# Kernel optimization log

Hardware: AMD Instinct MI355X
Metric: run time of the kernel (lower is better)

Reference implementation:

```python
import jax, jax.numpy as jnp
import numpy as np

B, N, C = 4, 1024, 1024
H, TD, MULT = 16, 256, 4
HD = C // H
MAX_LEN = 1024
EPS = 1e-5


def _layer_norm(x, g, b):
    m = jnp.mean(x, axis=-1, keepdims=True)
    v = jnp.mean((x - m) ** 2, axis=-1, keepdims=True)
    return (x - m) / jnp.sqrt(v + EPS) * g + b


def _skew(x):
    # x: [B,H,N,M] -> pad left on last dim, reshape, drop first row -> [B,H,N,M]
    b, h, n, m = x.shape
    x = jnp.pad(x, ((0, 0), (0, 0), (0, 0), (1, 0)))
    x = x.reshape(b, h, m + 1, n)
    return x[:, :, 1:, :]


def setup_inputs() -> dict:
    key = jax.random.key(0)
    ks = jax.random.split(key, 16)
    s = 0.02
    return {
        "x": jax.random.normal(ks[0], (B, N, C), jnp.float32),
        "t": jax.random.normal(ks[1], (B, TD), jnp.float32),
        "ln1_g": jnp.ones((C,), jnp.float32),
        "ln1_b": jnp.zeros((C,), jnp.float32),
        "qkv_w": jax.random.normal(ks[2], (C, 3 * C), jnp.float32) * s,
        "qkv_b": jnp.zeros((3 * C,), jnp.float32),
        "time_w": jax.random.normal(ks[3], (TD, 3 * C), jnp.float32) * s,
        "time_b": jnp.zeros((3 * C,), jnp.float32),
        "out_w": jax.random.normal(ks[4], (C, C), jnp.float32) * s,
        "out_b": jnp.zeros((C,), jnp.float32),
        "Er": jax.random.normal(ks[5], (MAX_LEN, HD), jnp.float32) * s,
        "ln2_g": jnp.ones((C,), jnp.float32),
        "ln2_b": jnp.zeros((C,), jnp.float32),
        "ff1_w": jax.random.normal(ks[6], (C, MULT * C), jnp.float32) * s,
        "ff1_b": jnp.zeros((MULT * C,), jnp.float32),
        "ff2_w": jax.random.normal(ks[7], (MULT * C, C), jnp.float32) * s,
        "ff2_b": jnp.zeros((C,), jnp.float32),
    }


def reference(x, t, ln1_g, ln1_b, qkv_w, qkv_b, time_w, time_b, out_w, out_b,
              Er, ln2_g, ln2_b, ff1_w, ff1_b, ff2_w, ff2_b):
    # ---- attention branch ----
    xn = _layer_norm(x, ln1_g, ln1_b)
    qkv = (xn @ qkv_w + qkv_b).reshape(B, N, 3, H, HD).transpose(2, 0, 3, 1, 4)
    q, k, v = qkv[0], qkv[1], qkv[2]  # [B,H,N,HD]
    tqkv = (t @ time_w + time_b).reshape(B, 1, 3, H, HD).transpose(2, 0, 3, 1, 4)
    q = q + tqkv[0]
    k = k + tqkv[1]
    v = v + tqkv[2]
    Er_n = Er[MAX_LEN - N:]  # [N,HD]
    rel = jnp.einsum('bhnd,md->bhnm', q, Er_n)
    rel = _skew(rel)
    scale = HD ** -0.5
    attn = jnp.einsum('bhnd,bhmd->bhnm', q, k) * scale + rel
    attn = jax.nn.softmax(attn, axis=-1)
    out = jnp.einsum('bhnm,bhmd->bhnd', attn, v)
    out = out.transpose(0, 2, 1, 3).reshape(B, N, C)
    x = x + (out @ out_w + out_b)
    # ---- FFN branch ----
    h = _layer_norm(x, ln2_g, ln2_b)
    h = jax.nn.gelu(h @ ff1_w + ff1_b, approximate=False)
    x = x + (h @ ff2_w + ff2_b)
    return x
```

## Files before the change

### kernel.cpp

```cpp
#include <hip/hip_runtime.h>
#include <hip/hip_bf16.h>

typedef __attribute__((ext_vector_type(8))) short short8;
typedef __attribute__((ext_vector_type(4))) float f32x4;
typedef __attribute__((ext_vector_type(16))) float f32x16;

#define DEV __device__ __forceinline__

DEV float bf2f(ushort u){ union { float f; unsigned int i; } x; x.i = ((unsigned int)u)<<16; return x.f; }
DEV ushort f2bf(float f){ union { float fl; unsigned int i; } x; x.fl = f; unsigned int r = x.i + 0x7fffu + ((x.i>>16)&1u); return (ushort)(r>>16); }

DEV void gl2lds16(const ushort* g, ushort* l){
  __builtin_amdgcn_global_load_lds((const __attribute__((address_space(1))) void*)g,
                                   (__attribute__((address_space(3))) void*)l, 16, 0, 0);
}
DEV f32x16 mfma32(short8 a, short8 b, f32x16 c){
  return __builtin_amdgcn_mfma_f32_32x32x16_bf16(a, b, c, 0, 0, 0);
}
DEV uint cvtpk(float lo, float hi){
  uint r; asm("v_cvt_pk_bf16_f32 %0, %1, %2" : "=v"(r) : "v"(lo), "v"(hi));
  return r;
}
DEV uint q8(float v){
  float c = fminf(fmaxf(v, -127.f), 127.f);
  return ((uint)(int)rintf(c)) & 255u;
}

__global__ void cvt_f2b(const float* __restrict__ in, ushort* __restrict__ out, int n){
  int i = blockIdx.x*blockDim.x + threadIdx.x;
  int stride = gridDim.x*blockDim.x;
  for (; i < n; i += stride) out[i] = f2bf(in[i]);
}

__global__ __launch_bounds__(256) void wt_cvt(const float* __restrict__ in, ushort* __restrict__ out,
                                              int K, int N, int ldk){
  const int n0 = blockIdx.x*64, k0 = blockIdx.y*64;
  __shared__ float T[64][65];
  const int tid = threadIdx.x;
  const int r = tid>>4, c = (tid&15)*4;
  #pragma unroll
  for (int p=0;p<4;p++){
    float4 v = *(const float4*)&in[(size_t)(k0 + p*16 + r)*N + n0 + c];
    T[p*16+r][c+0]=v.x; T[p*16+r][c+1]=v.y; T[p*16+r][c+2]=v.z; T[p*16+r][c+3]=v.w;
  }
  __syncthreads();
  #pragma unroll
  for (int p=0;p<4;p++){
    int n = p*16 + r;
    ushort u0 = f2bf(T[c+0][n]), u1 = f2bf(T[c+1][n]), u2 = f2bf(T[c+2][n]), u3 = f2bf(T[c+3][n]);
    ushort4 u = make_ushort4(u0,u1,u2,u3);
    *(ushort4*)&out[(size_t)(n0+n)*ldk + k0 + c] = u;
  }
}

__global__ __launch_bounds__(256) void vt_k(const ushort* __restrict__ qkv, ushort* __restrict__ vt){
  const int bh = blockIdx.y; const int b = bh>>4, h = bh&15;
  const int n0 = blockIdx.x*64;
  __shared__ ushort T[64][66];
  const int tid = threadIdx.x;
  const int r = tid>>3, c8 = (tid&7)*8;
  #pragma unroll
  for (int p=0;p<2;p++){
    int row = p*32 + r;
    short8 v = *(const short8*)&qkv[(size_t)(b*1024 + n0 + row)*3200 + 2048 + h*64 + c8];
    #pragma unroll
    for (int i=0;i<8;i++) T[row][c8+i] = ((ushort*)&v)[i];
  }
  __syncthreads();
  #pragma unroll
  for (int p=0;p<2;p++){
    int d = p*32 + r;
    union { ushort u[8]; short8 v; } o;
    #pragma unroll
    for (int i=0;i<8;i++) o.u[i] = T[c8+i][d];
    *(short8*)&vt[(size_t)(bh*64 + d)*1152 + n0 + c8] = o.v;
  }
}

__global__ __launch_bounds__(256) void ln_rows(const float* __restrict__ in,
                                               const float* __restrict__ g,
                                               const float* __restrict__ bta,
                                               ushort* __restrict__ out, int ldo){
  int row = blockIdx.x; int tid = threadIdx.x;
  const float* x = in + (size_t)row*1024;
  float v[4]; float s = 0.f;
  #pragma unroll
  for (int i=0;i<4;i++){ v[i] = x[tid + 256*i]; s += v[i]; }
  __shared__ float rbuf[256];
  rbuf[tid] = s; __syncthreads();
  for (int off=128; off>0; off>>=1){ if (tid<off) rbuf[tid]+=rbuf[tid+off]; __syncthreads(); }
  float mean = rbuf[0] * (1.f/1024.f);
  __syncthreads();
  float s2 = 0.f;
  #pragma unroll
  for (int i=0;i<4;i++){ float d=v[i]-mean; s2 += d*d; }
  rbuf[tid] = s2; __syncthreads();
  for (int off=128; off>0; off>>=1){ if (tid<off) rbuf[tid]+=rbuf[tid+off]; __syncthreads(); }
  float var = rbuf[0] * (1.f/1024.f);
  float rstd = rsqrtf(var + 1e-5f);
  #pragma unroll
  for (int i=0;i<4;i++){ int c = tid+256*i; out[(size_t)row*ldo+c] = f2bf((v[i]-mean)*rstd*g[c]+bta[c]); }
}

__global__ __launch_bounds__(256) void tq_gemm2(const float* __restrict__ t, const float* __restrict__ tw,
                                                const float* __restrict__ tb, float* __restrict__ tq){
  const int tid = threadIdx.x;
  const int j = blockIdx.x*64 + (tid & 63);
  const int sl = tid >> 6;
  float acc[4] = {0.f,0.f,0.f,0.f};
  for (int k = sl*64; k < sl*64+64; ++k){
    float wv = tw[(size_t)k*3072 + j];
    #pragma unroll
    for (int b=0;b<4;b++) acc[b] = fmaf(t[b*256+k], wv, acc[b]);
  }
  __shared__ float red[4][4][64];
  #pragma unroll
  for (int b=0;b<4;b++) red[sl][b][tid&63] = acc[b];
  __syncthreads();
  if (sl == 0){
    #pragma unroll
    for (int b=0;b<4;b++)
      tq[b*3072 + j] = red[0][b][tid&63] + red[1][b][tid&63] + red[2][b][tid&63] + red[3][b][tid&63] + tb[j];
  }
}

template<int EPI, int TN>
__global__ __launch_bounds__(256) void gemm4(
    const ushort* __restrict__ A, const ushort* __restrict__ Bt,
    const float* __restrict__ bias, const float* __restrict__ extra,
    ushort* __restrict__ outb, float* __restrict__ outf,
    int K, int lda, int ldb, int ldo, int lde, int nbx)
{
  constexpr int NJ = TN/32;
  __shared__ __align__(16) ushort Al[2][128*32];
  __shared__ __align__(16) ushort Bl[2][TN*32];
  const int nwg = gridDim.x, cpx = nwg >> 3;
  const int bid = blockIdx.x;
  const int swz = (bid & 7)*cpx + (bid >> 3);
  const int m0 = (swz / nbx)*128, n0 = (swz % nbx)*TN;
  const int tid = threadIdx.x, lane = tid & 63, wid = tid >> 6;
  const int wm = (wid&1)*64, wn = (wid>>1)*(TN/2);
  const int l15 = lane&15, l4 = lane>>4;
  f32x4 acc[4][NJ];
  #pragma unroll
  for (int i=0;i<4;i++)
    #pragma unroll
    for (int jx=0;jx<NJ;jx++){ acc[i][jx][0]=0.f; acc[i][jx][1]=0.f; acc[i][jx][2]=0.f; acc[i][jx][3]=0.f; }
  const ushort* a0p = A + (size_t)(m0 + (tid>>2))*lda + (tid&3)*8;
  const ushort* a1p = A + (size_t)(m0 + 64 + (tid>>2))*lda + (tid&3)*8;
  const ushort* b0p = Bt + (size_t)(n0 + (tid>>2))*ldb + (tid&3)*8;
  const ushort* b1p = nullptr;
  if constexpr (TN==128) b1p = Bt + (size_t)(n0 + 64 + (tid>>2))*ldb + (tid&3)*8;
  const int lsl = tid*8, lsh = (tid+256)*8;

  gl2lds16(a0p, &Al[0][lsl]);
  gl2lds16(a1p, &Al[0][lsh]);
  gl2lds16(b0p, &Bl[0][lsl]);
  if constexpr (TN==128) gl2lds16(b1p, &Bl[0][lsh]);
  __syncthreads();

  const int nk = K >> 5;
  for (int it=0; it<nk; ++it){
    const int cur = it & 1;
    ushort* Ac = Al[cur];  ushort* Bc = Bl[cur];
    if (it+1 < nk){
      const int k1 = (it+1) << 5;
      gl2lds16(a0p + k1, &Al[cur^1][lsl]);
      gl2lds16(a1p + k1, &Al[cur^1][lsh]);
      gl2lds16(b0p + k1, &Bl[cur^1][lsl]);
      if constexpr (TN==128) gl2lds16(b1p + k1, &Bl[cur^1][lsh]);
    }
    short8 af[4], bfr[NJ];
    #pragma unroll
    for (int mi=0;mi<4;mi++) af[mi]  = *(const short8*)&Ac[(wm + mi*16 + l15)*32 + l4*8];
    #pragma unroll
    for (int nj=0;nj<NJ;nj++) bfr[nj] = *(const short8*)&Bc[(wn + nj*16 + l15)*32 + l4*8];
    #pragma unroll
    for (int mi=0;mi<4;mi++)
      #pragma unroll
      for (int nj=0;nj<NJ;nj++)
        acc[mi][nj] = __builtin_amdgcn_mfma_f32_16x16x32_bf16(af[mi], bfr[nj], acc[mi][nj], 0,0,0);
    __syncthreads();
  }
  #pragma unroll
  for (int mi=0;mi<4;mi++)
    #pragma unroll
    for (int nj=0;nj<NJ;nj++)
      #pragma unroll
      for (int j=0;j<4;j++){
        int row = m0 + wm + mi*16 + l4*4 + j;
        int col = n0 + wn + nj*16 + l15;
        float v = acc[mi][nj][j] + bias[col];
        if constexpr (EPI==0){ v += extra[(size_t)(row>>10)*lde + col]; outb[(size_t)row*ldo+col] = f2bf(v); }
        else if constexpr (EPI==1){ v += extra[(size_t)row*lde + col]; outf[(size_t)row*ldo+col] = v; }
        else { v = 0.5f*v*(1.f+erff(v*0.70710678118f)); outb[(size_t)row*ldo+col] = f2bf(v); }
      }
}

__global__ __launch_bounds__(256) void relskew8_v3(
    const ushort* __restrict__ qkv, const ushort* __restrict__ Er,
    signed char* __restrict__ srel)
{
  const int bid0 = blockIdx.x;
  const int swz = (bid0 & 7)*256 + (bid0 >> 3);
  const int bh = swz >> 5, b = bh >> 4, h = bh & 15;
  const int r0 = (swz & 31)*32;
  const int tid = threadIdx.x, w = tid >> 6, lane = tid & 63;
  const int l31 = lane & 31, hi = lane >> 5;

  __shared__ signed char T8[33*1040];
  signed char* srb = srel + (size_t)bh*1024*1040;

  if (tid < 33){
    int tgt = r0 - 1 + tid;
    int c = tgt + 1;
    if (tgt >= 0 && c <= 1023) T8[tid*1040 + c] = 0;
  }

  const ushort* Qp = qkv + (size_t)b*1024*3200 + h*64;
  const int r = r0 + l31;
  short8 qf0 = *(const short8*)(Qp + (size_t)r*3200 +      hi*8);
  short8 qf1 = *(const short8*)(Qp + (size_t)r*3200 + 16 + hi*8);
  short8 qf2 = *(const short8*)(Qp + (size_t)r*3200 + 32 + hi*8);
  short8 qf3 = *(const short8*)(Qp + (size_t)r*3200 + 48 + hi*8);

  const float ESC = 92.332481f;
  for (int t=0; t<8; ++t){
    const int e0 = w*256 + t*32;
    const ushort* ep = Er + (size_t)(e0 + l31)*64 + hi*8;
    short8 ea0 = *(const short8*)(ep);
    short8 ea1 = *(const short8*)(ep + 16);
    short8 ea2 = *(const short8*)(ep + 32);
    short8 ea3 = *(const short8*)(ep + 48);
    f32x16 acc = {};
    acc = mfma32(ea0, qf0, acc);
    acc = mfma32(ea1, qf1, acc);
    acc = mfma32(ea2, qf2, acc);
    acc = mfma32(ea3, qf3, acc);
    #pragma unroll
    for (int q=0;q<4;q++)
      #pragma unroll
      for (int j=0;j<4;j++){
        int e = e0 + 8*q + 4*hi + j;
        signed char v = (signed char)(int)q8(acc[4*q+j]*ESC);
        bool below = (e + r) >= 1023;
        int i = below ? (l31 + 1) : l31;
        int c = e + r + (below ? -1023 : 1);
        T8[i*1040 + c] = v;
      }
  }
  __syncthreads();

  const int c4 = tid*4;
  #pragma unroll 4
  for (int i=0; i<33; ++i){
    int tgt = r0 - 1 + i;
    if (tgt < 0) continue;
    int lo = (i==0) ? (r0+1) : 0;
    int hh = (i==32) ? min(r0+32, 1023) : 1023;
    if (c4 >= lo && c4+3 <= hh){
      *(uint*)(srb + (size_t)tgt*1040 + c4) = *(const uint*)&T8[i*1040 + c4];
    } else if (c4 <= hh && c4+3 >= lo){
      #pragma unroll
      for (int k2=0;k2<4;k2++){
        int c = c4 + k2;
        if (c >= lo && c <= hh) srb[(size_t)tgt*1040 + c] = T8[i*1040 + c];
      }
    }
  }
}

__global__ __launch_bounds__(256) void attn9s(
    const ushort* __restrict__ qkv, const signed char* __restrict__ srel,
    const ushort* __restrict__ Vt, float* __restrict__ part)
{
  const int bid0 = blockIdx.x;
  const int swz = (bid0 & 7)*128 + (bid0 >> 3);
  const int bh = swz >> 4, b = bh >> 4, h = bh & 15;
  const int rblk = ((swz >> 1) & 7)*128;
  const int kvh = swz & 1;
  const int tid = threadIdx.x, w = tid >> 6, lane = tid & 63;
  const int l31 = lane & 31, hi = lane >> 5;
  const int r = rblk + w*32 + l31;
  const ushort* Qp = qkv + (size_t)b*1024*3200 + h*64;
  const ushort* Kp = Qp + 1024;
  const ushort* Vp = Vt + (size_t)bh*64*1152;
  const signed char* Bp = srel + (size_t)bh*1024*1040 + (size_t)r*1040 + hi*4;

  short8 qf0 = *(const short8*)(Qp + (size_t)r*3200 +      hi*8);
  short8 qf1 = *(const short8*)(Qp + (size_t)r*3200 + 16 + hi*8);
  short8 qf2 = *(const short8*)(Qp + (size_t)r*3200 + 32 + hi*8);
  short8 qf3 = *(const short8*)(Qp + (size_t)r*3200 + 48 + hi*8);

  f32x16 O0 = {}, O1 = {};
  float lsum = 0.f;

  const int t0 = kvh*16, tend = t0 + 15;
  short8 kA0 = *(const short8*)(Kp + (size_t)(t0*32 + l31)*3200 +      hi*8);
  short8 kA1 = *(const short8*)(Kp + (size_t)(t0*32 + l31)*3200 + 16 + hi*8);
  short8 kA2 = *(const short8*)(Kp + (size_t)(t0*32 + l31)*3200 + 32 + hi*8);
  short8 kA3 = *(const short8*)(Kp + (size_t)(t0*32 + l31)*3200 + 48 + hi*8);
  short8 kB0, kB1, kB2, kB3;

  auto step = [&](short8& ka0, short8& ka1, short8& ka2, short8& ka3,
                  short8& kn0, short8& kn1, short8& kn2, short8& kn3, int t){
    const int c0 = t*32;
    if (t < tend){
      const ushort* kp = Kp + (size_t)(c0 + 32 + l31)*3200 + hi*8;
      kn0 = *(const short8*)(kp);
      kn1 = *(const short8*)(kp + 16);
      kn2 = *(const short8*)(kp + 32);
      kn3 = *(const short8*)(kp + 48);
    }
    uint bw[4];
    #pragma unroll
    for (int rq=0;rq<4;rq++) bw[rq] = *(const uint*)(Bp + c0 + rq*8);
    short8 v00 = *(const short8*)(Vp + (size_t)l31*1152      + c0 +      hi*8);
    short8 v01 = *(const short8*)(Vp + (size_t)l31*1152      + c0 + 16 + hi*8);
    short8 v10 = *(const short8*)(Vp + (size_t)(32+l31)*1152 + c0 +      hi*8);
    short8 v11 = *(const short8*)(Vp + (size_t)(32+l31)*1152 + c0 + 16 + hi*8);
    f32x16 S = {};
    __builtin_amdgcn_s_setprio(1);
    S = mfma32(ka0, qf0, S);
    S = mfma32(ka1, qf1, S);
    S = mfma32(ka2, qf2, S);
    S = mfma32(ka3, qf3, S);
    __builtin_amdgcn_s_setprio(0);
    float p[16];
    float s0=0.f, s1=0.f, s2=0.f, s3=0.f;
    #pragma unroll
    for (int rq=0;rq<4;rq++)
      #pragma unroll
      for (int j=0;j<4;j++){
        float bias = (float)(signed char)((bw[rq] >> (8*j)) & 255u) * 0.015625f;
        float pv = __builtin_amdgcn_exp2f(fmaf(S[rq*4+j], 0.18033688f, bias));
        p[rq*4+j] = pv;
        if (j==0) s0 += pv; else if (j==1) s1 += pv; else if (j==2) s2 += pv; else s3 += pv;
      }
    lsum += (s0+s1)+(s2+s3);
    uint W00=cvtpk(p[0],p[1]),   W01=cvtpk(p[2],p[3]);
    uint W10=cvtpk(p[4],p[5]),   W11=cvtpk(p[6],p[7]);
    uint W20=cvtpk(p[8],p[9]),   W21=cvtpk(p[10],p[11]);
    uint W30=cvtpk(p[12],p[13]), W31=cvtpk(p[14],p[15]);
    uint x00 = (uint)__shfl_xor((int)(hi? W00 : W10), 32, 64);
    uint x01 = (uint)__shfl_xor((int)(hi? W01 : W11), 32, 64);
    uint x10 = (uint)__shfl_xor((int)(hi? W20 : W30), 32, 64);
    uint x11 = (uint)__shfl_xor((int)(hi? W21 : W31), 32, 64);
    union { uint u[4]; short8 v; } pf0, pf1;
    pf0.u[0] = hi ? x00 : W00;  pf0.u[1] = hi ? x01 : W01;
    pf0.u[2] = hi ? W10 : x00;  pf0.u[3] = hi ? W11 : x01;
    pf1.u[0] = hi ? x10 : W20;  pf1.u[1] = hi ? x11 : W21;
    pf1.u[2] = hi ? W30 : x10;  pf1.u[3] = hi ? W31 : x11;
    __builtin_amdgcn_s_setprio(1);
    O0 = mfma32(v00, pf0.v, O0);
    O0 = mfma32(v01, pf1.v, O0);
    O1 = mfma32(v10, pf0.v, O1);
    O1 = mfma32(v11, pf1.v, O1);
    __builtin_amdgcn_s_setprio(0);
  };
  for (int t=t0; t<t0+16; t+=2){
    step(kA0,kA1,kA2,kA3, kB0,kB1,kB2,kB3, t);
    step(kB0,kB1,kB2,kB3, kA0,kA1,kA2,kA3, t+1);
  }
  float lrow = lsum + __shfl_xor(lsum, 32, 64);

  float* pp = part + ((size_t)kvh*65536 + (size_t)bh*1024 + r)*68;
  #pragma unroll
  for (int rq=0;rq<4;rq++)
    #pragma unroll
    for (int s=0;s<2;s++){
      int reg = rq*4 + s*2;
      int d = rq*8 + hi*4 + s*2;
      *(float2*)(pp + d)      = make_float2(O0[reg], O0[reg+1]);
      *(float2*)(pp + 32 + d) = make_float2(O1[reg], O1[reg+1]);
    }
  if (hi == 0) pp[64] = lrow;
}

__global__ __launch_bounds__(256) void attn_merge(const float* __restrict__ part,
                                                  ushort* __restrict__ out){
  const int row = blockIdx.x*32 + (threadIdx.x>>3);
  const int dseg = (threadIdx.x&7)*8;
  const int bh = row>>10, rr = row&1023, b = bh>>4, h = bh&15;
  const float* p0 = part + (size_t)row*68;
  const float* p1 = part + ((size_t)65536 + row)*68;
  float inv = 1.f/(p0[64] + p1[64]);
  float4 a0 = *(const float4*)(p0 + dseg), a1 = *(const float4*)(p0 + dseg + 4);
  float4 b0 = *(const float4*)(p1 + dseg), b1 = *(const float4*)(p1 + dseg + 4);
  union { uint u[4]; short8 v; } ov;
  ov.u[0] = cvtpk((a0.x+b0.x)*inv, (a0.y+b0.y)*inv);
  ov.u[1] = cvtpk((a0.z+b0.z)*inv, (a0.w+b0.w)*inv);
  ov.u[2] = cvtpk((a1.x+b1.x)*inv, (a1.y+b1.y)*inv);
  ov.u[3] = cvtpk((a1.z+b1.z)*inv, (a1.w+b1.w)*inv);
  *(short8*)&out[((size_t)(b*1024 + rr))*1152 + h*64 + dseg] = ov.v;
}

extern "C" void kernel_launch(void* const* d_in, const int* in_sizes, int n_in,
                              void* d_out, int out_size, void* d_ws, size_t ws_size,
                              hipStream_t stream)
{
  const float* x    = (const float*)d_in[0];
  const float* t    = (const float*)d_in[1];
  const float* ln1g = (const float*)d_in[2];
  const float* ln1b = (const float*)d_in[3];
  const float* qkvw = (const float*)d_in[4];
  const float* qkvb = (const float*)d_in[5];
  const float* timew= (const float*)d_in[6];
  const float* timeb= (const float*)d_in[7];
  const float* outw = (const float*)d_in[8];
  const float* outbv= (const float*)d_in[9];
  const float* Er   = (const float*)d_in[10];
  const float* ln2g = (const float*)d_in[11];
  const float* ln2b = (const float*)d_in[12];
  const float* ff1w = (const float*)d_in[13];
  const float* ff1b = (const float*)d_in[14];
  const float* ff2w = (const float*)d_in[15];
  const float* ff2b = (const float*)d_in[16];
  float* o = (float*)d_out;

  char* ws = (char*)d_ws;
  ushort* qkvw_t = (ushort*)(ws);
  ushort* outw_t = (ushort*)(ws + 7077888);
  ushort* ff1w_t = (ushort*)(ws + 9437184);
  ushort* ff2w_t = (ushort*)(ws + 18874368);
  ushort* er_b   = (ushort*)(ws + 27525120);
  float*  tq     = (float*) (ws + 27656192);
  ushort* bufA   = (ushort*)(ws + 27705344);
  ushort* vt     = (ushort*)(ws + 37142528);
  ushort* bufB   = (ushort*)(ws + 46579712);
  signed char* srel8 = (signed char*)(ws + 81182720);
  float* part    = (float*)(ws + 150994944);

  wt_cvt<<<dim3(48,16),256,0,stream>>>(qkvw, qkvw_t, 1024, 3072, 1152);
  wt_cvt<<<dim3(16,16),256,0,stream>>>(outw, outw_t, 1024, 1024, 1152);
  wt_cvt<<<dim3(64,16),256,0,stream>>>(ff1w, ff1w_t, 1024, 4096, 1152);
  wt_cvt<<<dim3(16,64),256,0,stream>>>(ff2w, ff2w_t, 4096, 1024, 4224);
  cvt_f2b<<<256,256,0,stream>>>(Er, er_b, 65536);

  ln_rows<<<4096,256,0,stream>>>(x, ln1g, ln1b, bufA, 1152);
  tq_gemm2<<<48,256,0,stream>>>(t, timew, timeb, tq);
  gemm4<0,128><<<768,256,0,stream>>>(bufA, qkvw_t, qkvb, tq, bufB, nullptr,
                                     1024, 1152, 1152, 3200, 3072, 24);
  vt_k<<<dim3(16,64),256,0,stream>>>(bufB, vt);
  relskew8_v3<<<2048,256,0,stream>>>(bufB, er_b, srel8);
  attn9s<<<1024,256,0,stream>>>(bufB, srel8, vt, part);
  attn_merge<<<2048,256,0,stream>>>(part, bufA);
  gemm4<1,64><<<512,256,0,stream>>>(bufA, outw_t, outbv, x, nullptr, o,
                                    1024, 1152, 1152, 1024, 1024, 16);
  ln_rows<<<4096,256,0,stream>>>(o, ln2g, ln2b, bufA, 1152);
  gemm4<2,128><<<1024,256,0,stream>>>(bufA, ff1w_t, ff1b, nullptr, bufB, nullptr,
                                      1024, 1152, 1152, 4224, 0, 32);
  gemm4<1,64><<<512,256,0,stream>>>(bufB, ff2w_t, ff2b, o, nullptr, o,
                                    4096, 4224, 4224, 1024, 1024, 16);
}
```

Before: 391.5 us.

## Drop split-KV in attention, fuse normalization, prefetch V and bias

The attention kernel no longer splits the key range across two blocks. Each block now walks all 32 key tiles and normalizes and writes bf16 output directly, which removes the fp32 partial buffer and the separate merge kernel. V and the int8 bias are now double-buffered in registers alongside K, so their loads are issued one step ahead. The cost is half as many blocks (512), which means less parallelism on the GPU, plus more register pressure from the extra prefetch buffers.

```diff
diff --git a/kernel.cpp b/kernel.cpp
--- a/kernel.cpp
+++ b/kernel.cpp
@@ -270,21 +270,21 @@
   }
 }
 
-__global__ __launch_bounds__(256) void attn9s(
+__global__ __launch_bounds__(256) void attn10(
     const ushort* __restrict__ qkv, const signed char* __restrict__ srel,
-    const ushort* __restrict__ Vt, float* __restrict__ part)
+    const ushort* __restrict__ Vt, ushort* __restrict__ out)
 {
   const int bid0 = blockIdx.x;
-  const int swz = (bid0 & 7)*128 + (bid0 >> 3);
-  const int bh = swz >> 4, b = bh >> 4, h = bh & 15;
-  const int rblk = ((swz >> 1) & 7)*128;
-  const int kvh = swz & 1;
+  const int swz = (bid0 & 7)*64 + (bid0 >> 3);
+  const int bh = swz >> 3, b = bh >> 4, h = bh & 15;
+  const int rblk = (swz & 7)*128;
   const int tid = threadIdx.x, w = tid >> 6, lane = tid & 63;
   const int l31 = lane & 31, hi = lane >> 5;
   const int r = rblk + w*32 + l31;
   const ushort* Qp = qkv + (size_t)b*1024*3200 + h*64;
   const ushort* Kp = Qp + 1024;
-  const ushort* Vp = Vt + (size_t)bh*64*1152;
+  const ushort* Vp0 = Vt + (size_t)bh*64*1152 + (size_t)l31*1152 + hi*8;
+  const ushort* Vp1 = Vt + (size_t)bh*64*1152 + (size_t)(32+l31)*1152 + hi*8;
   const signed char* Bp = srel + (size_t)bh*1024*1040 + (size_t)r*1040 + hi*4;
 
   short8 qf0 = *(const short8*)(Qp + (size_t)r*3200 +      hi*8);
@@ -295,30 +295,44 @@
   f32x16 O0 = {}, O1 = {};
   float lsum = 0.f;
 
-  const int t0 = kvh*16, tend = t0 + 15;
-  short8 kA0 = *(const short8*)(Kp + (size_t)(t0*32 + l31)*3200 +      hi*8);
-  short8 kA1 = *(const short8*)(Kp + (size_t)(t0*32 + l31)*3200 + 16 + hi*8);
-  short8 kA2 = *(const short8*)(Kp + (size_t)(t0*32 + l31)*3200 + 32 + hi*8);
-  short8 kA3 = *(const short8*)(Kp + (size_t)(t0*32 + l31)*3200 + 48 + hi*8);
-  short8 kB0, kB1, kB2, kB3;
+  short8 kA0 = *(const short8*)(Kp + (size_t)l31*3200 +      hi*8);
+  short8 kA1 = *(const short8*)(Kp + (size_t)l31*3200 + 16 + hi*8);
+  short8 kA2 = *(const short8*)(Kp + (size_t)l31*3200 + 32 + hi*8);
+  short8 kA3 = *(const short8*)(Kp + (size_t)l31*3200 + 48 + hi*8);
+  short8 vA0 = *(const short8*)(Vp0);
+  short8 vA1 = *(const short8*)(Vp0 + 16);
+  short8 vA2 = *(const short8*)(Vp1);
+  short8 vA3 = *(const short8*)(Vp1 + 16);
+  uint bA0 = *(const uint*)(Bp);
+  uint bA1 = *(const uint*)(Bp + 8);
+  uint bA2 = *(const uint*)(Bp + 16);
+  uint bA3 = *(const uint*)(Bp + 24);
+  short8 kB0, kB1, kB2, kB3, vB0, vB1, vB2, vB3;
+  uint bB0, bB1, bB2, bB3;
 
   auto step = [&](short8& ka0, short8& ka1, short8& ka2, short8& ka3,
-                  short8& kn0, short8& kn1, short8& kn2, short8& kn3, int t){
+                  short8& va0, short8& va1, short8& va2, short8& va3,
+                  uint& ba0, uint& ba1, uint& ba2, uint& ba3,
+                  short8& kn0, short8& kn1, short8& kn2, short8& kn3,
+                  short8& vn0, short8& vn1, short8& vn2, short8& vn3,
+                  uint& bn0, uint& bn1, uint& bn2, uint& bn3, int t){
     const int c0 = t*32;
-    if (t < tend){
-      const ushort* kp = Kp + (size_t)(c0 + 32 + l31)*3200 + hi*8;
+    if (t < 31){
+      const int c1 = c0 + 32;
+      const ushort* kp = Kp + (size_t)(c1 + l31)*3200 + hi*8;
       kn0 = *(const short8*)(kp);
       kn1 = *(const short8*)(kp + 16);
       kn2 = *(const short8*)(kp + 32);
       kn3 = *(const short8*)(kp + 48);
+      vn0 = *(const short8*)(Vp0 + c1);
+      vn1 = *(const short8*)(Vp0 + c1 + 16);
+      vn2 = *(const short8*)(Vp1 + c1);
+      vn3 = *(const short8*)(Vp1 + c1 + 16);
+      bn0 = *(const uint*)(Bp + c1);
+      bn1 = *(const uint*)(Bp + c1 + 8);
+      bn2 = *(const uint*)(Bp + c1 + 16);
+      bn3 = *(const uint*)(Bp + c1 + 24);
     }
-    uint bw[4];
-    #pragma unroll
-    for (int rq=0;rq<4;rq++) bw[rq] = *(const uint*)(Bp + c0 + rq*8);
-    short8 v00 = *(const short8*)(Vp + (size_t)l31*1152      + c0 +      hi*8);
-    short8 v01 = *(const short8*)(Vp + (size_t)l31*1152      + c0 + 16 + hi*8);
-    short8 v10 = *(const short8*)(Vp + (size_t)(32+l31)*1152 + c0 +      hi*8);
-    short8 v11 = *(const short8*)(Vp + (size_t)(32+l31)*1152 + c0 + 16 + hi*8);
     f32x16 S = {};
     __builtin_amdgcn_s_setprio(1);
     S = mfma32(ka0, qf0, S);
@@ -327,6 +341,7 @@
     S = mfma32(ka3, qf3, S);
     __builtin_amdgcn_s_setprio(0);
     float p[16];
+    uint bw[4] = {ba0, ba1, ba2, ba3};
     float s0=0.f, s1=0.f, s2=0.f, s3=0.f;
     #pragma unroll
     for (int rq=0;rq<4;rq++)
@@ -352,47 +367,31 @@
     pf1.u[0] = hi ? x10 : W20;  pf1.u[1] = hi ? x11 : W21;
     pf1.u[2] = hi ? W30 : x10;  pf1.u[3] = hi ? W31 : x11;
     __builtin_amdgcn_s_setprio(1);
-    O0 = mfma32(v00, pf0.v, O0);
-    O0 = mfma32(v01, pf1.v, O0);
-    O1 = mfma32(v10, pf0.v, O1);
-    O1 = mfma32(v11, pf1.v, O1);
+    O0 = mfma32(va0, pf0.v, O0);
+    O0 = mfma32(va1, pf1.v, O0);
+    O1 = mfma32(va2, pf0.v, O1);
+    O1 = mfma32(va3, pf1.v, O1);
     __builtin_amdgcn_s_setprio(0);
   };
-  for (int t=t0; t<t0+16; t+=2){
-    step(kA0,kA1,kA2,kA3, kB0,kB1,kB2,kB3, t);
-    step(kB0,kB1,kB2,kB3, kA0,kA1,kA2,kA3, t+1);
-  }
-  float lrow = lsum + __shfl_xor(lsum, 32, 64);
-
-  float* pp = part + ((size_t)kvh*65536 + (size_t)bh*1024 + r)*68;
+  for (int t=0;t<32;t+=2){
+    step(kA0,kA1,kA2,kA3, vA0,vA1,vA2,vA3, bA0,bA1,bA2,bA3,
+         kB0,kB1,kB2,kB3, vB0,vB1,vB2,vB3, bB0,bB1,bB2,bB3, t);
+    step(kB0,kB1,kB2,kB3, vB0,vB1,vB2,vB3, bB0,bB1,bB2,bB3,
+         kA0,kA1,kA2,kA3, vA0,vA1,vA2,vA3, bA0,bA1,bA2,bA3, t+1);
+  }
+  float inv = 1.f/(lsum + __shfl_xor(lsum, 32, 64));
+  ushort* op = out + ((size_t)(b*1024 + r))*1152 + h*64;
   #pragma unroll
   for (int rq=0;rq<4;rq++)
     #pragma unroll
     for (int s=0;s<2;s++){
       int reg = rq*4 + s*2;
+      uint w0 = cvtpk(O0[reg]*inv, O0[reg+1]*inv);
+      uint w1 = cvtpk(O1[reg]*inv, O1[reg+1]*inv);
       int d = rq*8 + hi*4 + s*2;
-      *(float2*)(pp + d)      = make_float2(O0[reg], O0[reg+1]);
-      *(float2*)(pp + 32 + d) = make_float2(O1[reg], O1[reg+1]);
+      *(uint*)(op + d) = w0;
+      *(uint*)(op + 32 + d) = w1;
     }
-  if (hi == 0) pp[64] = lrow;
-}
-
-__global__ __launch_bounds__(256) void attn_merge(const float* __restrict__ part,
-                                                  ushort* __restrict__ out){
-  const int row = blockIdx.x*32 + (threadIdx.x>>3);
-  const int dseg = (threadIdx.x&7)*8;
-  const int bh = row>>10, rr = row&1023, b = bh>>4, h = bh&15;
-  const float* p0 = part + (size_t)row*68;
-  const float* p1 = part + ((size_t)65536 + row)*68;
-  float inv = 1.f/(p0[64] + p1[64]);
-  float4 a0 = *(const float4*)(p0 + dseg), a1 = *(const float4*)(p0 + dseg + 4);
-  float4 b0 = *(const float4*)(p1 + dseg), b1 = *(const float4*)(p1 + dseg + 4);
-  union { uint u[4]; short8 v; } ov;
-  ov.u[0] = cvtpk((a0.x+b0.x)*inv, (a0.y+b0.y)*inv);
-  ov.u[1] = cvtpk((a0.z+b0.z)*inv, (a0.w+b0.w)*inv);
-  ov.u[2] = cvtpk((a1.x+b1.x)*inv, (a1.y+b1.y)*inv);
-  ov.u[3] = cvtpk((a1.z+b1.z)*inv, (a1.w+b1.w)*inv);
-  *(short8*)&out[((size_t)(b*1024 + rr))*1152 + h*64 + dseg] = ov.v;
 }
 
 extern "C" void kernel_launch(void* const* d_in, const int* in_sizes, int n_in,
@@ -429,7 +428,6 @@
   ushort* vt     = (ushort*)(ws + 37142528);
   ushort* bufB   = (ushort*)(ws + 46579712);
   signed char* srel8 = (signed char*)(ws + 81182720);
-  float* part    = (float*)(ws + 150994944);
 
   wt_cvt<<<dim3(48,16),256,0,stream>>>(qkvw, qkvw_t, 1024, 3072, 1152);
   wt_cvt<<<dim3(16,16),256,0,stream>>>(outw, outw_t, 1024, 1024, 1152);
@@ -443,8 +441,7 @@
                                      1024, 1152, 1152, 3200, 3072, 24);
   vt_k<<<dim3(16,64),256,0,stream>>>(bufB, vt);
   relskew8_v3<<<2048,256,0,stream>>>(bufB, er_b, srel8);
-  attn9s<<<1024,256,0,stream>>>(bufB, srel8, vt, part);
-  attn_merge<<<2048,256,0,stream>>>(part, bufA);
+  attn10<<<512,256,0,stream>>>(bufB, srel8, vt, bufA);
   gemm4<1,64><<<512,256,0,stream>>>(bufA, outw_t, outbv, x, nullptr, o,
                                     1024, 1152, 1152, 1024, 1024, 16);
   ln_rows<<<4096,256,0,stream>>>(o, ln2g, ln2b, bufA, 1152);
```

New measurement: 374.9 us. -4.3%, faster.
